# Kernel optimization log

Hardware: AMD Instinct MI355X
Metric: run time of the kernel (lower is better)

Reference implementation:

```python
import jax, jax.numpy as jnp
import numpy as np

B, N, D = 4, 1024, 1024
H, HD, G = 16, 64, 4          # num_heads, dim_heads, num_groups
KVH = H // G                   # kv heads = 4


def setup_inputs() -> dict:
    key = jax.random.key(0)
    ks = jax.random.split(key, 5)
    s = 0.02
    return {
        "x": jax.random.normal(ks[0], (B, N, D), jnp.float32),
        "Wq": jax.random.normal(ks[1], (D, H * HD), jnp.float32) * s,
        "Wkv": jax.random.normal(ks[2], (D, 2 * H * HD // G), jnp.float32) * s,
        "Wg": jax.random.normal(ks[3], (D, H * HD), jnp.float32) * s,
        "bg": jnp.zeros((H * HD,), jnp.float32),
        "Wo": jax.random.normal(ks[4], (H * HD, D), jnp.float32) * s,
    }


def reference(x, Wq, Wkv, Wg, bg, Wo):
    # QKV projections (no bias on q/kv/o; bias on gate)
    q = (x @ Wq).reshape(B, N, H, HD).transpose(0, 2, 1, 3)        # (B,H,N,HD)
    kv = x @ Wkv                                                    # (B,N,2*KVH*HD)
    k, v = jnp.split(kv, 2, axis=-1)
    k = k.reshape(B, N, KVH, HD).transpose(0, 2, 1, 3)             # (B,KVH,N,HD)
    v = v.reshape(B, N, KVH, HD).transpose(0, 2, 1, 3)
    # GQA: repeat_interleave kv heads to match query heads
    k = jnp.repeat(k, G, axis=1)                                    # (B,H,N,HD)
    v = jnp.repeat(v, G, axis=1)
    # scaled dot product attention
    scores = jnp.einsum("bhqd,bhkd->bhqk", q, k) / jnp.sqrt(jnp.float32(HD))
    attn = jax.nn.softmax(scores, axis=-1)
    out = jnp.einsum("bhqk,bhkd->bhqd", attn, v)                    # (B,H,N,HD)
    out = out.transpose(0, 2, 1, 3).reshape(B, N, H * HD)
    # elementwise gate then output projection
    gate = x @ Wg + bg
    return (gate * out) @ Wo
```

## Files before the change

kernel.cpp:

```cpp
#include <hip/hip_runtime.h>
#include <hip/hip_bf16.h>
#include <stdint.h>

#define BB 4
#define NN 1024
#define DD 1024
#define HH 16
#define HDIM 64
#define KVHH 4
#define MM (BB * NN)

typedef __hip_bfloat16 bf16;
typedef __attribute__((ext_vector_type(8))) short bf16x8;
typedef __attribute__((ext_vector_type(4))) float f32x4;

__device__ __forceinline__ float b2f(unsigned short u) {
  return __uint_as_float(((unsigned)u) << 16);
}
__device__ __forceinline__ unsigned short f2b(float x) {
  bf16 h = __float2bfloat16(x);
  unsigned short u;
  __builtin_memcpy(&u, &h, 2);
  return u;
}
__device__ __forceinline__ f32x4 mfma16(bf16x8 a, bf16x8 b, f32x4 c) {
  return __builtin_amdgcn_mfma_f32_16x16x32_bf16(a, b, c, 0, 0, 0);
}
__device__ __forceinline__ void gl_lds16(const short* g, short* l) {
  __builtin_amdgcn_global_load_lds(
      (const __attribute__((address_space(1))) unsigned*)g,
      (__attribute__((address_space(3))) unsigned*)l, 16, 0, 0);
}

__global__ __launch_bounds__(256) void cvt_f32_bf16(const float* __restrict__ src,
                                                    short* __restrict__ dst, int n4) {
  int i = blockIdx.x * 256 + threadIdx.x;
  if (i < n4) {
    float4 v = *(const float4*)&src[(size_t)i * 4];
    ushort4 o;
    o.x = f2b(v.x); o.y = f2b(v.y); o.z = f2b(v.z); o.w = f2b(v.w);
    *(ushort4*)&dst[(size_t)i * 4] = o;
  }
}

__global__ __launch_bounds__(256) void transpose_all(
    const float* __restrict__ Wq, const float* __restrict__ Wkv,
    const float* __restrict__ Wg, const float* __restrict__ Wo,
    const float* __restrict__ bg, short* __restrict__ WcT,
    short* __restrict__ WoT, float* __restrict__ bias) {
  const int z = blockIdx.z;
  if (z == 4) {
    if (blockIdx.y == 0 && blockIdx.x < 10) {
      int i = blockIdx.x * 256 + threadIdx.x;
      if (i < 2560) bias[i] = (i >= 1024 && i < 2048) ? bg[i - 1024] : 0.f;
    }
    return;
  }
  const float* W;
  short* WT;
  int N = 1024;
  const int K = 1024;
  if (z == 0) { W = Wq; WT = WcT; }
  else if (z == 1) { W = Wg; WT = WcT + 1048576; }
  else if (z == 2) {
    W = Wkv; WT = WcT + 2097152; N = 512;
    if (blockIdx.x >= 8) return;
  } else { W = Wo; WT = WoT; }

  __shared__ short T[64 * 68];
  const int tid = threadIdx.x;
  const int n0 = blockIdx.x * 64, k0 = blockIdx.y * 64;
  {
    int i0 = tid >> 4, j4 = (tid & 15) * 4;
#pragma unroll
    for (int ii = 0; ii < 4; ++ii) {
      int i = i0 + 16 * ii;
      float4 w = *(const float4*)&W[(size_t)(k0 + i) * N + n0 + j4];
      ushort4 o;
      o.x = f2b(w.x); o.y = f2b(w.y); o.z = f2b(w.z); o.w = f2b(w.w);
      *(ushort4*)&T[i * 68 + j4] = o;
    }
  }
  __syncthreads();
  {
    int n = tid >> 2, k16 = (tid & 3) * 16;
    short tmp[16];
#pragma unroll
    for (int kk = 0; kk < 16; ++kk) tmp[kk] = T[(k16 + kk) * 68 + n];
    short* dst = WT + (size_t)(n0 + n) * K + k0 + k16;
#pragma unroll
    for (int s = 0; s < 16; s += 4) *(ushort4*)&dst[s] = *(const ushort4*)&tmp[s];
  }
}

__global__ __launch_bounds__(256) void gemm_proj(
    const short* __restrict__ A, const short* __restrict__ WT,
    const float* __restrict__ bias, short* __restrict__ qc,
    short* __restrict__ gc, short* __restrict__ kc, short* __restrict__ vt) {
  __shared__ short As[2][128 * 32];
  __shared__ short Bs[2][128 * 32];
  const int tid = threadIdx.x;
  const int wave = tid >> 6, lane = tid & 63, l15 = lane & 15, quad = lane >> 4;
  const int m0 = blockIdx.y * 128, n0 = blockIdx.x * 128;
  const int wm = (wave & 1) * 64, wn = (wave >> 1) * 64;
  const int arow = tid >> 2, ac = (tid & 3) * 8;
  const short* asrc = A + (size_t)(m0 + arow) * 1024 + ac;
  const short* bsrc = WT + (size_t)(n0 + arow) * 1024 + ac;

  gl_lds16(asrc, &As[0][wave * 512]);
  gl_lds16(asrc + 64 * 1024, &As[0][wave * 512 + 2048]);
  gl_lds16(bsrc, &Bs[0][wave * 512]);
  gl_lds16(bsrc + 64 * 1024, &Bs[0][wave * 512 + 2048]);

  f32x4 acc[4][4] = {};
  for (int k = 0; k < 32; ++k) {
    const int cur = k & 1;
    __syncthreads();
    if (k < 31) {
      const short* ap = asrc + (k + 1) * 32;
      const short* bp = bsrc + (k + 1) * 32;
      gl_lds16(ap, &As[1 - cur][wave * 512]);
      gl_lds16(ap + 64 * 1024, &As[1 - cur][wave * 512 + 2048]);
      gl_lds16(bp, &Bs[1 - cur][wave * 512]);
      gl_lds16(bp + 64 * 1024, &Bs[1 - cur][wave * 512 + 2048]);
    }
    bf16x8 af[4], bfr[4];
#pragma unroll
    for (int i = 0; i < 4; ++i)
      af[i] = *(const bf16x8*)&As[cur][(wm + 16 * i + l15) * 32 + quad * 8];
#pragma unroll
    for (int j = 0; j < 4; ++j)
      bfr[j] = *(const bf16x8*)&Bs[cur][(wn + 16 * j + l15) * 32 + quad * 8];
#pragma unroll
    for (int i = 0; i < 4; ++i)
#pragma unroll
      for (int j = 0; j < 4; ++j) acc[i][j] = mfma16(af[i], bfr[j], acc[i][j]);
  }
#pragma unroll
  for (int j = 0; j < 4; ++j) {
    int col = n0 + wn + 16 * j + l15;
    float bv = bias[col];
    int reg = col >> 6;
    int d = col & 63;
#pragma unroll
    for (int i = 0; i < 4; ++i) {
#pragma unroll
      for (int r = 0; r < 4; ++r) {
        int row = m0 + wm + 16 * i + quad * 4 + r;
        int b = row >> 10, tok = row & 1023;
        unsigned short v = f2b(acc[i][j][r] + bv);
        if (reg < 16)
          ((unsigned short*)qc)[((size_t)((b * 16 + reg) * 1024 + tok)) * 64 + d] = v;
        else if (reg < 32)
          ((unsigned short*)gc)[((size_t)((b * 16 + reg - 16) * 1024 + tok)) * 64 + d] = v;
        else if (reg < 36)
          ((unsigned short*)kc)[((size_t)((b * 4 + reg - 32) * 1024 + tok)) * 64 + d] = v;
        else
          ((unsigned short*)vt)[((size_t)((b * 4 + reg - 36) * 64 + d)) * 1024 + tok] = v;
      }
    }
  }
}

__global__ __launch_bounds__(256) void gemm_out(
    const short* __restrict__ A, const short* __restrict__ WT,
    float* __restrict__ Cout) {
  __shared__ short As[2][64 * 32];
  __shared__ short Bs[2][128 * 32];
  const int tid = threadIdx.x;
  const int wave = tid >> 6, lane = tid & 63, l15 = lane & 15, quad = lane >> 4;
  const int m0 = blockIdx.y * 64, n0 = blockIdx.x * 128;
  const int wm = (wave & 1) * 32, wn = (wave >> 1) * 64;
  const int arow = tid >> 2, ac = (tid & 3) * 8;
  const short* asrc = A + (size_t)(m0 + arow) * 1024 + ac;
  const short* bsrc = WT + (size_t)(n0 + arow) * 1024 + ac;

  gl_lds16(asrc, &As[0][wave * 512]);
  gl_lds16(bsrc, &Bs[0][wave * 512]);
  gl_lds16(bsrc + 64 * 1024, &Bs[0][wave * 512 + 2048]);

  f32x4 acc[2][4] = {};
  for (int k = 0; k < 32; ++k) {
    const int cur = k & 1;
    __syncthreads();
    if (k < 31) {
      const short* ap = asrc + (k + 1) * 32;
      const short* bp = bsrc + (k + 1) * 32;
      gl_lds16(ap, &As[1 - cur][wave * 512]);
      gl_lds16(bp, &Bs[1 - cur][wave * 512]);
      gl_lds16(bp + 64 * 1024, &Bs[1 - cur][wave * 512 + 2048]);
    }
    bf16x8 af[2], bfr[4];
#pragma unroll
    for (int i = 0; i < 2; ++i)
      af[i] = *(const bf16x8*)&As[cur][(wm + 16 * i + l15) * 32 + quad * 8];
#pragma unroll
    for (int j = 0; j < 4; ++j)
      bfr[j] = *(const bf16x8*)&Bs[cur][(wn + 16 * j + l15) * 32 + quad * 8];
#pragma unroll
    for (int i = 0; i < 2; ++i)
#pragma unroll
      for (int j = 0; j < 4; ++j) acc[i][j] = mfma16(af[i], bfr[j], acc[i][j]);
  }
#pragma unroll
  for (int j = 0; j < 4; ++j) {
    int col = n0 + wn + 16 * j + l15;
#pragma unroll
    for (int i = 0; i < 2; ++i) {
#pragma unroll
      for (int r = 0; r < 4; ++r) {
        int row = m0 + wm + 16 * i + quad * 4 + r;
        Cout[(size_t)row * 1024 + col] = acc[i][j][r];
      }
    }
  }
}

__global__ __launch_bounds__(256, 3) void attn_mfma4(
    const short* __restrict__ qc, const short* __restrict__ gc,
    const short* __restrict__ kc, const short* __restrict__ vt,
    unsigned short* __restrict__ gated) {
  __shared__ short Kt[2][64 * 64];
  __shared__ short Vt[2][64 * 64];
  __shared__ short Ps[64 * 64];
  __shared__ float Lpart[4 * 64];
  __shared__ float Lq[64];
  const int tid = threadIdx.x;
  const int w = tid >> 6, lane = tid & 63, l15 = lane & 15, quad = lane >> 4;
  const int qt = blockIdx.x, bh = blockIdx.y, b = bh >> 4, h = bh & 15, kvh = h >> 2;
  const int fs = l15 & 7;
  const int s0 = (quad ^ fs) * 8;
  const int s1 = ((4 + quad) ^ fs) * 8;

  bf16x8 qf[4][2];
#pragma unroll
  for (int jq = 0; jq < 4; ++jq) {
    const short* qp =
        qc + ((size_t)((b * 16 + h) * 1024) + qt * 64 + 16 * jq + l15) * 64 + quad * 8;
    qf[jq][0] = *(const bf16x8*)qp;
    qf[jq][1] = *(const bf16x8*)(qp + 32);
  }

  const int srow = lane >> 3;
  const int schunk = (lane & 7) ^ srow;
  const short* kstage = kc + ((size_t)((b * 4 + kvh) * 1024) + 16 * w + srow) * 64 + schunk * 8;
  const short* vstage = vt + ((size_t)((b * 4 + kvh) * 64) + 16 * w + srow) * 1024 + schunk * 8;

  f32x4 oacc[4];
  float ls[4];
#pragma unroll
  for (int jq = 0; jq < 4; ++jq) {
    oacc[jq] = (f32x4){0.f, 0.f, 0.f, 0.f};
    ls[jq] = 0.f;
  }

  const int pslot = ((2 * w + (quad >> 1)) ^ fs) * 8 + (quad & 1) * 4;

  gl_lds16(kstage, &Kt[0][(16 * w) * 64]);
  gl_lds16(kstage + 512, &Kt[0][(16 * w + 8) * 64]);
  gl_lds16(vstage, &Vt[0][(16 * w) * 64]);
  gl_lds16(vstage + 8192, &Vt[0][(16 * w + 8) * 64]);

  for (int kt = 0; kt < 16; ++kt) {
    const int cur = kt & 1;
    __syncthreads();
    bf16x8 kf0 = *(const bf16x8*)&Kt[cur][(16 * w + l15) * 64 + s0];
    bf16x8 kf1 = *(const bf16x8*)&Kt[cur][(16 * w + l15) * 64 + s1];
#pragma unroll
    for (int jq = 0; jq < 4; ++jq) {
      f32x4 st = mfma16(kf0, qf[jq][0], (f32x4){0.f, 0.f, 0.f, 0.f});
      st = mfma16(kf1, qf[jq][1], st);
      float p0 = __expf(st[0] * 0.125f);
      float p1 = __expf(st[1] * 0.125f);
      float p2 = __expf(st[2] * 0.125f);
      float p3 = __expf(st[3] * 0.125f);
      ls[jq] += (p0 + p1) + (p2 + p3);
      uint2 dd;
      dd.x = (unsigned)f2b(p0) | ((unsigned)f2b(p1) << 16);
      dd.y = (unsigned)f2b(p2) | ((unsigned)f2b(p3) << 16);
      *(uint2*)&Ps[(16 * jq + l15) * 64 + pslot] = dd;
    }
    __syncthreads();
    if (kt < 15) {
      const short* kp = kstage + (size_t)(kt + 1) * 4096;
      const short* vp = vstage + (size_t)(kt + 1) * 64;
      gl_lds16(kp, &Kt[1 - cur][(16 * w) * 64]);
      gl_lds16(kp + 512, &Kt[1 - cur][(16 * w + 8) * 64]);
      gl_lds16(vp, &Vt[1 - cur][(16 * w) * 64]);
      gl_lds16(vp + 8192, &Vt[1 - cur][(16 * w + 8) * 64]);
    }
    bf16x8 vf0 = *(const bf16x8*)&Vt[cur][(16 * w + l15) * 64 + s0];
    bf16x8 vf1 = *(const bf16x8*)&Vt[cur][(16 * w + l15) * 64 + s1];
#pragma unroll
    for (int jq = 0; jq < 4; ++jq) {
      bf16x8 pf0 = *(const bf16x8*)&Ps[(16 * jq + l15) * 64 + s0];
      bf16x8 pf1 = *(const bf16x8*)&Ps[(16 * jq + l15) * 64 + s1];
      oacc[jq] = mfma16(pf0, vf0, oacc[jq]);
      oacc[jq] = mfma16(pf1, vf1, oacc[jq]);
    }
  }

#pragma unroll
  for (int jq = 0; jq < 4; ++jq) {
    ls[jq] += __shfl_xor(ls[jq], 16);
    ls[jq] += __shfl_xor(ls[jq], 32);
  }
  if (quad == 0) {
#pragma unroll
    for (int jq = 0; jq < 4; ++jq) Lpart[w * 64 + 16 * jq + l15] = ls[jq];
  }
  __syncthreads();
  if (tid < 64)
    Lq[tid] = Lpart[tid] + Lpart[64 + tid] + Lpart[128 + tid] + Lpart[192 + tid];
  __syncthreads();

#pragma unroll
  for (int jq = 0; jq < 4; ++jq) {
#pragma unroll
    for (int r = 0; r < 4; ++r) {
      int qloc = 16 * jq + 4 * quad + r;
      float lv = Lq[qloc];
      float gv = b2f(((const unsigned short*)gc)[
          ((size_t)((b * 16 + h) * 1024) + qt * 64 + qloc) * 64 + 16 * w + l15]);
      size_t row = (size_t)(b * NN + qt * 64 + qloc);
      gated[row * 1024 + h * 64 + 16 * w + l15] = f2b(oacc[jq][r] / lv * gv);
    }
  }
}

extern "C" void kernel_launch(void* const* d_in, const int* in_sizes, int n_in,
                              void* d_out, int out_size, void* d_ws,
                              size_t ws_size, hipStream_t stream) {
  const float* x = (const float*)d_in[0];
  const float* Wq = (const float*)d_in[1];
  const float* Wkv = (const float*)d_in[2];
  const float* Wg = (const float*)d_in[3];
  const float* bg = (const float*)d_in[4];
  const float* Wo = (const float*)d_in[5];
  float* out = (float*)d_out;

  short* ws = (short*)d_ws;
  short* xb = ws;
  short* WcT = xb + 4194304;
  short* WoT = WcT + 2621440;
  short* qc = WoT + 1048576;
  short* gc = qc + 4194304;
  short* kc = gc + 4194304;
  short* vtw = kc + 1048576;
  float* bias_f32 = (float*)(vtw + 1048576);

  dim3 blk(256);
  cvt_f32_bf16<<<4096, blk, 0, stream>>>(x, xb, 1048576);
  transpose_all<<<dim3(16, 16, 5), blk, 0, stream>>>(Wq, Wkv, Wg, Wo, bg, WcT,
                                                     WoT, bias_f32);
  gemm_proj<<<dim3(20, 32), blk, 0, stream>>>(xb, WcT, bias_f32, qc, gc, kc, vtw);
  attn_mfma4<<<dim3(16, 64), blk, 0, stream>>>(qc, gc, kc, vtw, (unsigned short*)xb);
  gemm_out<<<dim3(8, 64), blk, 0, stream>>>(xb, WoT, out);
}
```

Baseline: 193.3 us.

## Fold x conversion into transpose kernel, shrink GEMM tiles, single-buffer attention

```diff
diff --git a/kernel.cpp b/kernel.cpp
--- a/kernel.cpp
+++ b/kernel.cpp
@@ -32,27 +32,29 @@
       (__attribute__((address_space(3))) unsigned*)l, 16, 0, 0);
 }
 
-__global__ __launch_bounds__(256) void cvt_f32_bf16(const float* __restrict__ src,
-                                                    short* __restrict__ dst, int n4) {
-  int i = blockIdx.x * 256 + threadIdx.x;
-  if (i < n4) {
-    float4 v = *(const float4*)&src[(size_t)i * 4];
-    ushort4 o;
-    o.x = f2b(v.x); o.y = f2b(v.y); o.z = f2b(v.z); o.w = f2b(v.w);
-    *(ushort4*)&dst[(size_t)i * 4] = o;
-  }
-}
-
 __global__ __launch_bounds__(256) void transpose_all(
     const float* __restrict__ Wq, const float* __restrict__ Wkv,
     const float* __restrict__ Wg, const float* __restrict__ Wo,
-    const float* __restrict__ bg, short* __restrict__ WcT,
-    short* __restrict__ WoT, float* __restrict__ bias) {
+    const float* __restrict__ bg, const float* __restrict__ x,
+    short* __restrict__ WcT, short* __restrict__ WoT,
+    float* __restrict__ bias, short* __restrict__ xb) {
   const int z = blockIdx.z;
   if (z == 4) {
     if (blockIdx.y == 0 && blockIdx.x < 10) {
       int i = blockIdx.x * 256 + threadIdx.x;
       if (i < 2560) bias[i] = (i >= 1024 && i < 2048) ? bg[i - 1024] : 0.f;
+    }
+    return;
+  }
+  if (z == 5) {
+    int base = (blockIdx.y * 16 + blockIdx.x) * 256 + threadIdx.x;
+#pragma unroll
+    for (int it = 0; it < 16; ++it) {
+      int i = base + it * 65536;
+      float4 v = *(const float4*)&x[(size_t)i * 4];
+      ushort4 o;
+      o.x = f2b(v.x); o.y = f2b(v.y); o.z = f2b(v.z); o.w = f2b(v.w);
+      *(ushort4*)&xb[(size_t)i * 4] = o;
     }
     return;
   }
@@ -93,26 +95,25 @@
   }
 }
 
-__global__ __launch_bounds__(256) void gemm_proj(
+__global__ __launch_bounds__(256, 5) void gemm_proj(
     const short* __restrict__ A, const short* __restrict__ WT,
     const float* __restrict__ bias, short* __restrict__ qc,
     short* __restrict__ gc, short* __restrict__ kc, short* __restrict__ vt) {
-  __shared__ short As[2][128 * 32];
+  __shared__ short As[2][64 * 32];
   __shared__ short Bs[2][128 * 32];
   const int tid = threadIdx.x;
   const int wave = tid >> 6, lane = tid & 63, l15 = lane & 15, quad = lane >> 4;
-  const int m0 = blockIdx.y * 128, n0 = blockIdx.x * 128;
-  const int wm = (wave & 1) * 64, wn = (wave >> 1) * 64;
+  const int m0 = blockIdx.y * 64, n0 = blockIdx.x * 128;
+  const int wm = (wave & 1) * 32, wn = (wave >> 1) * 64;
   const int arow = tid >> 2, ac = (tid & 3) * 8;
   const short* asrc = A + (size_t)(m0 + arow) * 1024 + ac;
   const short* bsrc = WT + (size_t)(n0 + arow) * 1024 + ac;
 
   gl_lds16(asrc, &As[0][wave * 512]);
-  gl_lds16(asrc + 64 * 1024, &As[0][wave * 512 + 2048]);
   gl_lds16(bsrc, &Bs[0][wave * 512]);
   gl_lds16(bsrc + 64 * 1024, &Bs[0][wave * 512 + 2048]);
 
-  f32x4 acc[4][4] = {};
+  f32x4 acc[2][4] = {};
   for (int k = 0; k < 32; ++k) {
     const int cur = k & 1;
     __syncthreads();
@@ -120,19 +121,18 @@
       const short* ap = asrc + (k + 1) * 32;
       const short* bp = bsrc + (k + 1) * 32;
       gl_lds16(ap, &As[1 - cur][wave * 512]);
-      gl_lds16(ap + 64 * 1024, &As[1 - cur][wave * 512 + 2048]);
       gl_lds16(bp, &Bs[1 - cur][wave * 512]);
       gl_lds16(bp + 64 * 1024, &Bs[1 - cur][wave * 512 + 2048]);
     }
-    bf16x8 af[4], bfr[4];
-#pragma unroll
-    for (int i = 0; i < 4; ++i)
+    bf16x8 af[2], bfr[4];
+#pragma unroll
+    for (int i = 0; i < 2; ++i)
       af[i] = *(const bf16x8*)&As[cur][(wm + 16 * i + l15) * 32 + quad * 8];
 #pragma unroll
     for (int j = 0; j < 4; ++j)
       bfr[j] = *(const bf16x8*)&Bs[cur][(wn + 16 * j + l15) * 32 + quad * 8];
 #pragma unroll
-    for (int i = 0; i < 4; ++i)
+    for (int i = 0; i < 2; ++i)
 #pragma unroll
       for (int j = 0; j < 4; ++j) acc[i][j] = mfma16(af[i], bfr[j], acc[i][j]);
   }
@@ -143,7 +143,7 @@
     int reg = col >> 6;
     int d = col & 63;
 #pragma unroll
-    for (int i = 0; i < 4; ++i) {
+    for (int i = 0; i < 2; ++i) {
 #pragma unroll
       for (int r = 0; r < 4; ++r) {
         int row = m0 + wm + 16 * i + quad * 4 + r;
@@ -162,48 +162,44 @@
   }
 }
 
-__global__ __launch_bounds__(256) void gemm_out(
+__global__ __launch_bounds__(256, 4) void gemm_out(
     const short* __restrict__ A, const short* __restrict__ WT,
     float* __restrict__ Cout) {
   __shared__ short As[2][64 * 32];
-  __shared__ short Bs[2][128 * 32];
+  __shared__ short Bs[2][64 * 32];
   const int tid = threadIdx.x;
   const int wave = tid >> 6, lane = tid & 63, l15 = lane & 15, quad = lane >> 4;
-  const int m0 = blockIdx.y * 64, n0 = blockIdx.x * 128;
-  const int wm = (wave & 1) * 32, wn = (wave >> 1) * 64;
+  const int m0 = blockIdx.y * 64, n0 = blockIdx.x * 64;
+  const int wm = (wave & 1) * 32, wn = (wave >> 1) * 32;
   const int arow = tid >> 2, ac = (tid & 3) * 8;
   const short* asrc = A + (size_t)(m0 + arow) * 1024 + ac;
   const short* bsrc = WT + (size_t)(n0 + arow) * 1024 + ac;
 
   gl_lds16(asrc, &As[0][wave * 512]);
   gl_lds16(bsrc, &Bs[0][wave * 512]);
-  gl_lds16(bsrc + 64 * 1024, &Bs[0][wave * 512 + 2048]);
-
-  f32x4 acc[2][4] = {};
+
+  f32x4 acc[2][2] = {};
   for (int k = 0; k < 32; ++k) {
     const int cur = k & 1;
     __syncthreads();
     if (k < 31) {
-      const short* ap = asrc + (k + 1) * 32;
-      const short* bp = bsrc + (k + 1) * 32;
-      gl_lds16(ap, &As[1 - cur][wave * 512]);
-      gl_lds16(bp, &Bs[1 - cur][wave * 512]);
-      gl_lds16(bp + 64 * 1024, &Bs[1 - cur][wave * 512 + 2048]);
-    }
-    bf16x8 af[2], bfr[4];
+      gl_lds16(asrc + (k + 1) * 32, &As[1 - cur][wave * 512]);
+      gl_lds16(bsrc + (k + 1) * 32, &Bs[1 - cur][wave * 512]);
+    }
+    bf16x8 af[2], bfr[2];
 #pragma unroll
     for (int i = 0; i < 2; ++i)
       af[i] = *(const bf16x8*)&As[cur][(wm + 16 * i + l15) * 32 + quad * 8];
 #pragma unroll
-    for (int j = 0; j < 4; ++j)
+    for (int j = 0; j < 2; ++j)
       bfr[j] = *(const bf16x8*)&Bs[cur][(wn + 16 * j + l15) * 32 + quad * 8];
 #pragma unroll
     for (int i = 0; i < 2; ++i)
 #pragma unroll
-      for (int j = 0; j < 4; ++j) acc[i][j] = mfma16(af[i], bfr[j], acc[i][j]);
-  }
-#pragma unroll
-  for (int j = 0; j < 4; ++j) {
+      for (int j = 0; j < 2; ++j) acc[i][j] = mfma16(af[i], bfr[j], acc[i][j]);
+  }
+#pragma unroll
+  for (int j = 0; j < 2; ++j) {
     int col = n0 + wn + 16 * j + l15;
 #pragma unroll
     for (int i = 0; i < 2; ++i) {
@@ -216,12 +212,12 @@
   }
 }
 
-__global__ __launch_bounds__(256, 3) void attn_mfma4(
+__global__ __launch_bounds__(256, 6) void attn_mfma5(
     const short* __restrict__ qc, const short* __restrict__ gc,
     const short* __restrict__ kc, const short* __restrict__ vt,
     unsigned short* __restrict__ gated) {
-  __shared__ short Kt[2][64 * 64];
-  __shared__ short Vt[2][64 * 64];
+  __shared__ short Kt[64 * 64];
+  __shared__ short Vt[64 * 64];
   __shared__ short Ps[64 * 64];
   __shared__ float Lpart[4 * 64];
   __shared__ float Lq[64];
@@ -256,16 +252,19 @@
 
   const int pslot = ((2 * w + (quad >> 1)) ^ fs) * 8 + (quad & 1) * 4;
 
-  gl_lds16(kstage, &Kt[0][(16 * w) * 64]);
-  gl_lds16(kstage + 512, &Kt[0][(16 * w + 8) * 64]);
-  gl_lds16(vstage, &Vt[0][(16 * w) * 64]);
-  gl_lds16(vstage + 8192, &Vt[0][(16 * w + 8) * 64]);
-
   for (int kt = 0; kt < 16; ++kt) {
-    const int cur = kt & 1;
-    __syncthreads();
-    bf16x8 kf0 = *(const bf16x8*)&Kt[cur][(16 * w + l15) * 64 + s0];
-    bf16x8 kf1 = *(const bf16x8*)&Kt[cur][(16 * w + l15) * 64 + s1];
+    __syncthreads();
+    {
+      const short* kp = kstage + (size_t)kt * 4096;
+      const short* vp = vstage + (size_t)kt * 64;
+      gl_lds16(kp, &Kt[(16 * w) * 64]);
+      gl_lds16(kp + 512, &Kt[(16 * w + 8) * 64]);
+      gl_lds16(vp, &Vt[(16 * w) * 64]);
+      gl_lds16(vp + 8192, &Vt[(16 * w + 8) * 64]);
+    }
+    __syncthreads();
+    bf16x8 kf0 = *(const bf16x8*)&Kt[(16 * w + l15) * 64 + s0];
+    bf16x8 kf1 = *(const bf16x8*)&Kt[(16 * w + l15) * 64 + s1];
 #pragma unroll
     for (int jq = 0; jq < 4; ++jq) {
       f32x4 st = mfma16(kf0, qf[jq][0], (f32x4){0.f, 0.f, 0.f, 0.f});
@@ -281,16 +280,8 @@
       *(uint2*)&Ps[(16 * jq + l15) * 64 + pslot] = dd;
     }
     __syncthreads();
-    if (kt < 15) {
-      const short* kp = kstage + (size_t)(kt + 1) * 4096;
-      const short* vp = vstage + (size_t)(kt + 1) * 64;
-      gl_lds16(kp, &Kt[1 - cur][(16 * w) * 64]);
-      gl_lds16(kp + 512, &Kt[1 - cur][(16 * w + 8) * 64]);
-      gl_lds16(vp, &Vt[1 - cur][(16 * w) * 64]);
-      gl_lds16(vp + 8192, &Vt[1 - cur][(16 * w + 8) * 64]);
-    }
-    bf16x8 vf0 = *(const bf16x8*)&Vt[cur][(16 * w + l15) * 64 + s0];
-    bf16x8 vf1 = *(const bf16x8*)&Vt[cur][(16 * w + l15) * 64 + s1];
+    bf16x8 vf0 = *(const bf16x8*)&Vt[(16 * w + l15) * 64 + s0];
+    bf16x8 vf1 = *(const bf16x8*)&Vt[(16 * w + l15) * 64 + s1];
 #pragma unroll
     for (int jq = 0; jq < 4; ++jq) {
       bf16x8 pf0 = *(const bf16x8*)&Ps[(16 * jq + l15) * 64 + s0];
@@ -350,10 +341,9 @@
   float* bias_f32 = (float*)(vtw + 1048576);
 
   dim3 blk(256);
-  cvt_f32_bf16<<<4096, blk, 0, stream>>>(x, xb, 1048576);
-  transpose_all<<<dim3(16, 16, 5), blk, 0, stream>>>(Wq, Wkv, Wg, Wo, bg, WcT,
-                                                     WoT, bias_f32);
-  gemm_proj<<<dim3(20, 32), blk, 0, stream>>>(xb, WcT, bias_f32, qc, gc, kc, vtw);
-  attn_mfma4<<<dim3(16, 64), blk, 0, stream>>>(qc, gc, kc, vtw, (unsigned short*)xb);
-  gemm_out<<<dim3(8, 64), blk, 0, stream>>>(xb, WoT, out);
-}
+  transpose_all<<<dim3(16, 16, 6), blk, 0, stream>>>(Wq, Wkv, Wg, Wo, bg, x,
+                                                     WcT, WoT, bias_f32, xb);
+  gemm_proj<<<dim3(20, 64), blk, 0, stream>>>(xb, WcT, bias_f32, qc, gc, kc, vtw);
+  attn_mfma5<<<dim3(16, 64), blk, 0, stream>>>(qc, gc, kc, vtw, (unsigned short*)xb);
+  gemm_out<<<dim3(16, 64), blk, 0, stream>>>(xb, WoT, out);
+}
```

Measured after the change: 190.6 us. Within noise of the previous version (-1.4%).
